# Kernel optimization log

Hardware: AMD Instinct MI355X
Metric: run time of the kernel (lower is better)

## Reference

```python
import jax, jax.numpy as jnp
import numpy as np
from jax import lax

GAMMA = 1.0
INF = 1000000.0  # matches the TF code's pseudo-infinity


def _pairwise_sq_dists(a, b):
    # ||a_i - b_j||^2 = ||a||^2 + ||b||^2 - 2 a.b ; avoids the [B,N,M,d] diff tensor
    a2 = jnp.sum(a * a, axis=-1)                      # (B, N)
    b2 = jnp.sum(b * b, axis=-1)                      # (B, M)
    ab = jnp.einsum('bnd,bmd->bnm', a, b)             # (B, N, M)
    return a2[:, :, None] + b2[:, None, :] - 2.0 * ab


def _soft_dtw(seq_a, seq_b, gamma):
    D = _pairwise_sq_dists(seq_a, seq_b)              # (B, N, M)
    B, N, M = D.shape
    dtype = D.dtype
    # row 0 of the DP table: R[0,0]=0, R[0,j>0]=INF
    row0 = jnp.full((B, M + 1), INF, dtype=dtype).at[:, 0].set(0.0)

    def row_step(prev_row, d_i):
        # prev_row: (B, M+1) = R[i-1, :]; d_i: (B, M) = D[:, i-1, :]
        def col_step(left, inputs):
            diag, up, d = inputs                      # each (B,)
            r = jnp.stack([diag, up, left], axis=-1)  # (B, 3)
            softmin = -gamma * jax.nn.logsumexp(-r / gamma, axis=-1)
            val = d + softmin
            return val, val
        left0 = jnp.full((B,), INF, dtype=dtype)      # R[i, 0] = INF
        xs = (prev_row[:, :-1].T, prev_row[:, 1:].T, d_i.T)  # scan over M
        _, vals = lax.scan(col_step, left0, xs)       # (M, B)
        new_row = jnp.concatenate([jnp.full((B, 1), INF, dtype=dtype), vals.T], axis=1)
        return new_row, None

    final_row, _ = lax.scan(row_step, row0, jnp.moveaxis(D, 1, 0))
    return final_row[:, -1]                           # R[N, M]


def setup_inputs() -> dict:
    key = jax.random.key(0)
    k1, k2 = jax.random.split(key)
    B, N, M, d = 128, 384, 384, 128
    seq_a = jax.random.normal(k1, (B, N, d), dtype=jnp.float32)
    seq_b = jax.random.normal(k2, (B, M, d), dtype=jnp.float32)
    return {"seq_a": seq_a, "seq_b": seq_b}


def reference(seq_a, seq_b):
    dist = _soft_dtw(seq_a, seq_b, GAMMA)
    return dist[:, None]                              # (B, 1)
```

## Files before the change

### kernel.cpp

```cpp
#include <hip/hip_runtime.h>
#include <stdint.h>

#define BATCH 128
#define SEQN  384
#define SEQM  384
#define DIM   128
#define KINF   1000000.0f
#define LOG2E  1.4426950408889634f
#define LN2    0.6931471805599453f
#define KINF2  (KINF * LOG2E)

#define RING    204
#define RSTRIDE 392

#define EXP2F(x) __builtin_amdgcn_exp2f(x)
#define LOG2F(x) __builtin_amdgcn_logf(x)

#define WG __HIP_MEMORY_SCOPE_WORKGROUP

typedef __attribute__((ext_vector_type(8))) short bf16x8;
typedef __attribute__((ext_vector_type(4))) float f32x4;

__device__ __forceinline__ unsigned short bf16_rne(float x) {
    uint32_t u = __float_as_uint(x);
    u += 0x7FFFu + ((u >> 16) & 1u);
    return (unsigned short)(u >> 16);
}
__device__ __forceinline__ uint32_t bf16_pair(float x, float y) {
    uint32_t ux = __float_as_uint(x); ux += 0x7FFFu + ((ux >> 16) & 1u);
    uint32_t uy = __float_as_uint(y); uy += 0x7FFFu + ((uy >> 16) & 1u);
    return (ux >> 16) | (uy & 0xFFFF0000u);
}

__device__ __forceinline__ float dpp_shfl_up1(float x) {
    return __int_as_float(__builtin_amdgcn_update_dpp(
        0, (int)__float_as_uint(x), 0x138 , 0xF, 0xF, false));
}

union frag_u { bf16x8 v; uint32_t u[4]; };

__global__ __launch_bounds__(512) void fused_dtw(
        const float* __restrict__ A, const float* __restrict__ B,
        float* __restrict__ out) {
    __shared__ __align__(16) unsigned short ring[RING * RSTRIDE];
    __shared__ __align__(16) float normA[SEQN];
    __shared__ int prod_done[16];
    __shared__ int cons_sl;

    const int bat  = blockIdx.x;
    const int tid  = threadIdx.x;
    const int wv   = tid >> 6;
    const int lane = tid & 63;

    if (tid < 16) prod_done[tid] = 0;
    if (tid == 16) cons_sl = -1;
    __syncthreads();

    if (wv == 4) {
        int g = 0;
        while (__hip_atomic_load(&cons_sl, __ATOMIC_ACQUIRE, WG) < 248) {
            __builtin_amdgcn_s_sleep(8);
            if (++g > (1 << 20)) break;
        }
        uint32_t pv = bf16_pair(KINF2, KINF2);
        #pragma unroll
        for (int c = 0; c < 4; c++) {
            uint32_t* p = (uint32_t*)&ring[(384 - RING + c) * RSTRIDE + 6 * lane];
            p[0] = pv; p[1] = pv; p[2] = pv;
        }
        if (lane == 0)
            __hip_atomic_fetch_add(&prod_done[12], 6, __ATOMIC_RELEASE, WG);
        return;
    }

    if (wv != 0) {
        const int pidx  = (wv < 4) ? (wv - 1) : (wv - 2);
        const int sbase = pidx * 4;
        const int l16 = lane & 15, q = lane >> 4;
        const float* __restrict__ Ab = A + (long)bat * SEQN * DIM;
        const float* __restrict__ Bb = B + (long)bat * SEQM * DIM;
        bool first = true;
        for (int k = 0; k < 12; k++) {
            if (k >= 6) {
                int thr = 32 * k - 110, g = 0;
                while (__hip_atomic_load(&cons_sl, __ATOMIC_ACQUIRE, WG) < thr) {
                    __builtin_amdgcn_s_sleep(2);
                    if (++g > (1 << 21)) break;
                }
            }
            frag_u bfrag[2][4];
            float bn[2];
            #pragma unroll
            for (int jg = 0; jg < 2; jg++) {
                const float* bp = Bb + (long)(32 * k + jg * 16 + l16) * DIM + q * 8;
                float s = 0.0f;
                #pragma unroll
                for (int kk = 0; kk < 4; kk++) {
                    float4 v0 = *(const float4*)(bp + kk * 32);
                    float4 v1 = *(const float4*)(bp + kk * 32 + 4);
                    bfrag[jg][kk].u[0] = bf16_pair(v0.x, v0.y);
                    bfrag[jg][kk].u[1] = bf16_pair(v0.z, v0.w);
                    bfrag[jg][kk].u[2] = bf16_pair(v1.x, v1.y);
                    bfrag[jg][kk].u[3] = bf16_pair(v1.z, v1.w);
                    s += v0.x*v0.x + v0.y*v0.y + v0.z*v0.z + v0.w*v0.w
                       + v1.x*v1.x + v1.y*v1.y + v1.z*v1.z + v1.w*v1.w;
                }
                s += __shfl_xor(s, 16, 64);
                s += __shfl_xor(s, 32, 64);
                bn[jg] = s;
            }
            float4 c0v[4], c1v[4];
            {
                const float* ap = Ab + (long)(sbase * 16 + l16) * DIM + q * 8;
                #pragma unroll
                for (int kk = 0; kk < 4; kk++) {
                    c0v[kk] = *(const float4*)(ap + kk * 32);
                    c1v[kk] = *(const float4*)(ap + kk * 32 + 4);
                }
            }
            #pragma unroll
            for (int s4 = 0; s4 < 4; s4++) {
                const int si = sbase + s4;
                float4 n0[4], n1[4];
                if (s4 < 3) {
                    const float* ap = Ab + (long)((si + 1) * 16 + l16) * DIM + q * 8;
                    #pragma unroll
                    for (int kk = 0; kk < 4; kk++) {
                        n0[kk] = *(const float4*)(ap + kk * 32);
                        n1[kk] = *(const float4*)(ap + kk * 32 + 4);
                    }
                }
                frag_u afr[4];
                #pragma unroll
                for (int kk = 0; kk < 4; kk++) {
                    afr[kk].u[0] = bf16_pair(c0v[kk].x, c0v[kk].y);
                    afr[kk].u[1] = bf16_pair(c0v[kk].z, c0v[kk].w);
                    afr[kk].u[2] = bf16_pair(c1v[kk].x, c1v[kk].y);
                    afr[kk].u[3] = bf16_pair(c1v[kk].z, c1v[kk].w);
                }
                if (first) {
                    float sa = 0.0f;
                    #pragma unroll
                    for (int kk = 0; kk < 4; kk++)
                        sa += c0v[kk].x*c0v[kk].x + c0v[kk].y*c0v[kk].y
                            + c0v[kk].z*c0v[kk].z + c0v[kk].w*c0v[kk].w
                            + c1v[kk].x*c1v[kk].x + c1v[kk].y*c1v[kk].y
                            + c1v[kk].z*c1v[kk].z + c1v[kk].w*c1v[kk].w;
                    sa += __shfl_xor(sa, 16, 64);
                    sa += __shfl_xor(sa, 32, 64);
                    if (q == 0) normA[si * 16 + l16] = sa;
                }
                f32x4 acc0 = {0.0f, 0.0f, 0.0f, 0.0f};
                f32x4 acc1 = {0.0f, 0.0f, 0.0f, 0.0f};
                #pragma unroll
                for (int kk = 0; kk < 4; kk++) {
                    acc0 = __builtin_amdgcn_mfma_f32_16x16x32_bf16(
                               afr[kk].v, bfrag[0][kk].v, acc0, 0, 0, 0);
                    acc1 = __builtin_amdgcn_mfma_f32_16x16x32_bf16(
                               afr[kk].v, bfrag[1][kk].v, acc1, 0, 0, 0);
                }
                if (first) asm volatile("s_waitcnt lgkmcnt(0)" ::: "memory");
                float4 an = *(const float4*)&normA[si * 16 + q * 4];
                #pragma unroll
                for (int jg = 0; jg < 2; jg++) {
                    int col  = 32 * k + jg * 16 + l16;
                    int slot = col >= RING ? col - RING : col;
                    f32x4 ac = jg ? acc1 : acc0;
                    ushort4 pk;
                    pk.x = bf16_rne((an.x + bn[jg] - 2.0f * ac[0]) * LOG2E);
                    pk.y = bf16_rne((an.y + bn[jg] - 2.0f * ac[1]) * LOG2E);
                    pk.z = bf16_rne((an.z + bn[jg] - 2.0f * ac[2]) * LOG2E);
                    pk.w = bf16_rne((an.w + bn[jg] - 2.0f * ac[3]) * LOG2E);
                    *(ushort4*)&ring[slot * RSTRIDE + si * 16 + q * 4] = pk;
                }
                if (s4 < 3) {
                    #pragma unroll
                    for (int kk = 0; kk < 4; kk++) { c0v[kk] = n0[kk]; c1v[kk] = n1[kk]; }
                }
            }
            first = false;
            if (lane == 0)
                __hip_atomic_fetch_add(&prod_done[k], 1, __ATOMIC_RELEASE, WG);
        }
        return;
    }

    const int t = lane;
    {
        int g = 0;
        while (__hip_atomic_load(&prod_done[0], __ATOMIC_ACQUIRE, WG) < 6)
            if (++g > (1 << 22)) break;
    }
    __builtin_amdgcn_s_setprio(1);
    const unsigned short* __restrict__ ringT = ring + 6 * t;

    float prev[6];
    #pragma unroll
    for (int r = 0; r < 6; r++) prev[r] = KINF2;

    uint3 dslot[4];
    #pragma unroll
    for (int j = 0; j < 4; j++) {
        int c = j - t;
        int cc = c < 0 ? 0 : c;
        dslot[j] = *(const uint3*)(ringT + (long)cc * RSTRIDE);
    }

    float rcv_up = KINF2, rcv_diag = KINF2;
    float lane0_diag = 0.0f;
    const bool isl0 = (t == 0);
    int kdone = 0;

#define UNPACK(d, w)                                                        \
    d[0] = __uint_as_float(w.x << 16);                                      \
    d[1] = __uint_as_float(w.x & 0xFFFF0000u);                              \
    d[2] = __uint_as_float(w.y << 16);                                      \
    d[3] = __uint_as_float(w.y & 0xFFFF0000u);                              \
    d[4] = __uint_as_float(w.z << 16);                                      \
    d[5] = __uint_as_float(w.z & 0xFFFF0000u);

#define COLPASS(dX, diag0, upseed, LEFTV, NEWV)                             \
    {                                                                       \
        float Bp = (upseed), Fp = 1.0f;                                     \
        float Bv[6], Fv[6];                                                 \
        _Pragma("unroll")                                                   \
        for (int r = 0; r < 6; r++) {                                       \
            float vd = (r == 0) ? (diag0) : LEFTV[r - 1];                   \
            float vl = LEFTV[r];                                            \
            float m3 = fminf(fminf(vd, vl), Bp);            \
            float al = EXP2F(m3 - Bp);                                      \
            float be = EXP2F(m3 - vd) + EXP2F(m3 - vl);                     \
            float Fr = __builtin_fmaf(al, Fp, be);                          \
            float Br = dX[r] + m3;                                          \
            Bv[r] = Br; Fv[r] = Fr;                                         \
            Bp = Br; Fp = Fr;                                               \
        }                                                                   \
        _Pragma("unroll")                                                   \
        for (int r = 0; r < 6; r++)                                         \
            NEWV[r] = Bv[r] - LOG2F(Fv[r]);                                 \
    }

#define SLOT(J, S)                                                          \
    {                                                                       \
        uint3 w = dslot[J];                                                 \
        {   int cn = (S) + 4 - t;                                           \
            int cc = cn < 0 ? 0 : (cn > 387 ? 387 : cn);                    \
            int sl = cc >= RING ? cc - RING : cc;                           \
            dslot[J] = *(const uint3*)(ringT + (long)sl * RSTRIDE);         \
        }                                                                   \
        float d6[6];                                                        \
        UNPACK(d6, w)                                                       \
        float dg = isl0 ? lane0_diag : rcv_diag;                            \
        float up = isl0 ? KINF2 : rcv_up;                                   \
        COLPASS(d6, dg, up, prev, prev)                                     \
        rcv_diag = rcv_up;                                                  \
        rcv_up = dpp_shfl_up1(prev[5]);                                     \
        lane0_diag = KINF2;                                                 \
    }

    for (int i = 0; i < 111; i++) {
        int kr = (4 * i + 7) >> 5;
        if (kr > 12) kr = 12;
        if (kr > kdone) {
            int g = 0;
            while (__hip_atomic_load(&prod_done[kr], __ATOMIC_ACQUIRE, WG) < 6)
                if (++g > (1 << 22)) break;
            kdone = kr;
        }
        SLOT(0, 4 * i)
        SLOT(1, 4 * i + 1)
        SLOT(2, 4 * i + 2)
        SLOT(3, 4 * i + 3)
        if ((i & 1) && t == 0)
            __hip_atomic_store(&cons_sl, 4 * i + 3,
                               __ATOMIC_RELEASE, WG);
    }
    SLOT(0, 444)
    SLOT(1, 445)
    SLOT(2, 446)
#undef SLOT
#undef COLPASS
#undef UNPACK

    if (t == 63) out[bat] = prev[5] * LN2;
}

extern "C" void kernel_launch(void* const* d_in, const int* in_sizes, int n_in,
                              void* d_out, int out_size, void* d_ws, size_t ws_size,
                              hipStream_t stream) {
    (void)in_sizes; (void)n_in; (void)out_size; (void)d_ws; (void)ws_size;
    const float* a = (const float*)d_in[0];
    const float* b = (const float*)d_in[1];
    float* out = (float*)d_out;

    fused_dtw<<<dim3(BATCH), dim3(512), 0, stream>>>(a, b, out);
}
```

Measured before the change: 184.0 us.

## Pack two batch items per workgroup with separate producer/consumer pipelines and smaller ring

```diff
diff --git a/kernel.cpp b/kernel.cpp
--- a/kernel.cpp
+++ b/kernel.cpp
@@ -10,7 +10,7 @@
 #define LN2    0.6931471805599453f
 #define KINF2  (KINF * LOG2E)
 
-#define RING    204
+#define RING    100
 #define RSTRIDE 392
 
 #define EXP2F(x) __builtin_amdgcn_exp2f(x)
@@ -42,48 +42,36 @@
 __global__ __launch_bounds__(512) void fused_dtw(
         const float* __restrict__ A, const float* __restrict__ B,
         float* __restrict__ out) {
-    __shared__ __align__(16) unsigned short ring[RING * RSTRIDE];
-    __shared__ __align__(16) float normA[SEQN];
-    __shared__ int prod_done[16];
-    __shared__ int cons_sl;
-
-    const int bat  = blockIdx.x;
+    __shared__ __align__(16) unsigned short ring[2][RING * RSTRIDE];
+    __shared__ __align__(16) float normA[2][SEQN];
+    __shared__ int prod_done[2][16];
+    __shared__ int cons_sl[2];
+
+    const int bx   = blockIdx.x;
     const int tid  = threadIdx.x;
     const int wv   = tid >> 6;
     const int lane = tid & 63;
 
-    if (tid < 16) prod_done[tid] = 0;
-    if (tid == 16) cons_sl = -1;
+    if (tid < 32) prod_done[tid >> 4][tid & 15] = 0;
+    if (tid == 32) cons_sl[0] = -1;
+    if (tid == 33) cons_sl[1] = -1;
     __syncthreads();
 
-    if (wv == 4) {
-        int g = 0;
-        while (__hip_atomic_load(&cons_sl, __ATOMIC_ACQUIRE, WG) < 248) {
-            __builtin_amdgcn_s_sleep(8);
-            if (++g > (1 << 20)) break;
-        }
-        uint32_t pv = bf16_pair(KINF2, KINF2);
-        #pragma unroll
-        for (int c = 0; c < 4; c++) {
-            uint32_t* p = (uint32_t*)&ring[(384 - RING + c) * RSTRIDE + 6 * lane];
-            p[0] = pv; p[1] = pv; p[2] = pv;
-        }
-        if (lane == 0)
-            __hip_atomic_fetch_add(&prod_done[12], 6, __ATOMIC_RELEASE, WG);
-        return;
-    }
-
-    if (wv != 0) {
-        const int pidx  = (wv < 4) ? (wv - 1) : (wv - 2);
-        const int sbase = pidx * 4;
+    const int b   = wv >> 2;
+    const int bat = 2 * bx + b;
+
+    if ((wv & 3) != 0) {
+        const int pidx  = (wv & 3) - 1;
+        const int sbase = pidx * 8;
         const int l16 = lane & 15, q = lane >> 4;
         const float* __restrict__ Ab = A + (long)bat * SEQN * DIM;
         const float* __restrict__ Bb = B + (long)bat * SEQM * DIM;
+        unsigned short* __restrict__ rng = ring[b];
         bool first = true;
         for (int k = 0; k < 12; k++) {
-            if (k >= 6) {
-                int thr = 32 * k - 110, g = 0;
-                while (__hip_atomic_load(&cons_sl, __ATOMIC_ACQUIRE, WG) < thr) {
+            if (k >= 3) {
+                int thr = 32 * k - 9, g = 0;
+                while (__hip_atomic_load(&cons_sl[b], __ATOMIC_ACQUIRE, WG) < thr) {
                     __builtin_amdgcn_s_sleep(2);
                     if (++g > (1 << 21)) break;
                 }
@@ -119,10 +107,10 @@
                 }
             }
             #pragma unroll
-            for (int s4 = 0; s4 < 4; s4++) {
-                const int si = sbase + s4;
+            for (int s8 = 0; s8 < 8; s8++) {
+                const int si = sbase + s8;
                 float4 n0[4], n1[4];
-                if (s4 < 3) {
+                if (s8 < 7) {
                     const float* ap = Ab + (long)((si + 1) * 16 + l16) * DIM + q * 8;
                     #pragma unroll
                     for (int kk = 0; kk < 4; kk++) {
@@ -148,7 +136,7 @@
                             + c1v[kk].z*c1v[kk].z + c1v[kk].w*c1v[kk].w;
                     sa += __shfl_xor(sa, 16, 64);
                     sa += __shfl_xor(sa, 32, 64);
-                    if (q == 0) normA[si * 16 + l16] = sa;
+                    if (q == 0) normA[b][si * 16 + l16] = sa;
                 }
                 f32x4 acc0 = {0.0f, 0.0f, 0.0f, 0.0f};
                 f32x4 acc1 = {0.0f, 0.0f, 0.0f, 0.0f};
@@ -160,27 +148,44 @@
                                afr[kk].v, bfrag[1][kk].v, acc1, 0, 0, 0);
                 }
                 if (first) asm volatile("s_waitcnt lgkmcnt(0)" ::: "memory");
-                float4 an = *(const float4*)&normA[si * 16 + q * 4];
+                float4 an = *(const float4*)&normA[b][si * 16 + q * 4];
                 #pragma unroll
                 for (int jg = 0; jg < 2; jg++) {
-                    int col  = 32 * k + jg * 16 + l16;
-                    int slot = col >= RING ? col - RING : col;
+                    int col = 32 * k + jg * 16 + l16;
+                    int sl  = col;
+                    if (sl >= 200) sl -= 200;
+                    if (sl >= 100) sl -= 100;
                     f32x4 ac = jg ? acc1 : acc0;
                     ushort4 pk;
                     pk.x = bf16_rne((an.x + bn[jg] - 2.0f * ac[0]) * LOG2E);
                     pk.y = bf16_rne((an.y + bn[jg] - 2.0f * ac[1]) * LOG2E);
                     pk.z = bf16_rne((an.z + bn[jg] - 2.0f * ac[2]) * LOG2E);
                     pk.w = bf16_rne((an.w + bn[jg] - 2.0f * ac[3]) * LOG2E);
-                    *(ushort4*)&ring[slot * RSTRIDE + si * 16 + q * 4] = pk;
-                }
-                if (s4 < 3) {
+                    *(ushort4*)&rng[sl * RSTRIDE + si * 16 + q * 4] = pk;
+                }
+                if (s8 < 7) {
                     #pragma unroll
                     for (int kk = 0; kk < 4; kk++) { c0v[kk] = n0[kk]; c1v[kk] = n1[kk]; }
                 }
             }
             first = false;
             if (lane == 0)
-                __hip_atomic_fetch_add(&prod_done[k], 1, __ATOMIC_RELEASE, WG);
+                __hip_atomic_fetch_add(&prod_done[b][k], 1, __ATOMIC_RELEASE, WG);
+        }
+        if (pidx == 0) {
+            int g = 0;
+            while (__hip_atomic_load(&cons_sl[b], __ATOMIC_ACQUIRE, WG) < 352) {
+                __builtin_amdgcn_s_sleep(8);
+                if (++g > (1 << 20)) break;
+            }
+            uint32_t pv = bf16_pair(KINF2, KINF2);
+            #pragma unroll
+            for (int c = 0; c < 4; c++) {
+                uint32_t* p = (uint32_t*)&rng[(84 + c) * RSTRIDE + 6 * lane];
+                p[0] = pv; p[1] = pv; p[2] = pv;
+            }
+            if (lane == 0)
+                __hip_atomic_store(&prod_done[b][12], 3, __ATOMIC_RELEASE, WG);
         }
         return;
     }
@@ -188,11 +193,11 @@
     const int t = lane;
     {
         int g = 0;
-        while (__hip_atomic_load(&prod_done[0], __ATOMIC_ACQUIRE, WG) < 6)
+        while (__hip_atomic_load(&prod_done[b][0], __ATOMIC_ACQUIRE, WG) < 3)
             if (++g > (1 << 22)) break;
     }
     __builtin_amdgcn_s_setprio(1);
-    const unsigned short* __restrict__ ringT = ring + 6 * t;
+    const unsigned short* __restrict__ ringT = ring[b] + 6 * t;
 
     float prev[6];
     #pragma unroll
@@ -245,9 +250,13 @@
         uint3 w = dslot[J];                                                 \
         {   int cn = (S) + 4 - t;                                           \
             int cc = cn < 0 ? 0 : (cn > 387 ? 387 : cn);                    \
-            int sl = cc >= RING ? cc - RING : cc;                           \
+            int sl = cc;                                                    \
+            if (sl >= 200) sl -= 200;                                       \
+            if (sl >= 100) sl -= 100;                                       \
             dslot[J] = *(const uint3*)(ringT + (long)sl * RSTRIDE);         \
         }                                                                   \
+        if (isl0)                             \
+            __hip_atomic_store(&cons_sl[b], (S), __ATOMIC_RELAXED, WG);     \
         float d6[6];                                                        \
         UNPACK(d6, w)                                                       \
         float dg = isl0 ? lane0_diag : rcv_diag;                            \
@@ -263,7 +272,7 @@
         if (kr > 12) kr = 12;
         if (kr > kdone) {
             int g = 0;
-            while (__hip_atomic_load(&prod_done[kr], __ATOMIC_ACQUIRE, WG) < 6)
+            while (__hip_atomic_load(&prod_done[b][kr], __ATOMIC_ACQUIRE, WG) < 3)
                 if (++g > (1 << 22)) break;
             kdone = kr;
         }
@@ -272,8 +281,7 @@
         SLOT(2, 4 * i + 2)
         SLOT(3, 4 * i + 3)
         if ((i & 1) && t == 0)
-            __hip_atomic_store(&cons_sl, 4 * i + 3,
-                               __ATOMIC_RELEASE, WG);
+            __hip_atomic_store(&cons_sl[b], 4 * i + 3, __ATOMIC_RELEASE, WG);
     }
     SLOT(0, 444)
     SLOT(1, 445)
@@ -293,5 +301,5 @@
     const float* b = (const float*)d_in[1];
     float* out = (float*)d_out;
 
-    fused_dtw<<<dim3(BATCH), dim3(512), 0, stream>>>(a, b, out);
-}
+    fused_dtw<<<dim3(BATCH / 2), dim3(512), 0, stream>>>(a, b, out);
+}
```

Measured after the change: 316.3 us. 72.0% more time.

## Carry soft-DTW cells as (base, mantissa) pairs to drop per-cell log2

Applied to the files above, without the earlier changes.

```diff
diff --git a/kernel.cpp b/kernel.cpp
--- a/kernel.cpp
+++ b/kernel.cpp
@@ -194,9 +194,9 @@
     __builtin_amdgcn_s_setprio(1);
     const unsigned short* __restrict__ ringT = ring + 6 * t;
 
-    float prev[6];
+    float prevB[6], prevF[6];
     #pragma unroll
-    for (int r = 0; r < 6; r++) prev[r] = KINF2;
+    for (int r = 0; r < 6; r++) { prevB[r] = KINF2; prevF[r] = 1.0f; }
 
     uint3 dslot[4];
     #pragma unroll
@@ -206,8 +206,9 @@
         dslot[j] = *(const uint3*)(ringT + (long)cc * RSTRIDE);
     }
 
-    float rcv_up = KINF2, rcv_diag = KINF2;
-    float lane0_diag = 0.0f;
+    float upB = KINF2, upF = 1.0f;
+    float dgB = KINF2, dgF = 1.0f;
+    float l0dB = 0.0f, l0dF = 1.0f;
     const bool isl0 = (t == 0);
     int kdone = 0;
 
@@ -219,25 +220,26 @@
     d[4] = __uint_as_float(w.z << 16);                                      \
     d[5] = __uint_as_float(w.z & 0xFFFF0000u);
 
-#define COLPASS(dX, diag0, upseed, LEFTV, NEWV)                             \
+#define COLPASS(dX, dgB_, dgF_, upB_, upF_)                                 \
     {                                                                       \
-        float Bp = (upseed), Fp = 1.0f;                                     \
-        float Bv[6], Fv[6];                                                 \
+        float Bp = (upB_), Fp = (upF_);                                     \
+        float cdB = (dgB_), cdF = (dgF_);                                   \
         _Pragma("unroll")                                                   \
         for (int r = 0; r < 6; r++) {                                       \
-            float vd = (r == 0) ? (diag0) : LEFTV[r - 1];                   \
-            float vl = LEFTV[r];                                            \
-            float m3 = fminf(fminf(vd, vl), Bp);            \
-            float al = EXP2F(m3 - Bp);                                      \
-            float be = EXP2F(m3 - vd) + EXP2F(m3 - vl);                     \
-            float Fr = __builtin_fmaf(al, Fp, be);                          \
+            float vdB = cdB, vdF = cdF;                                     \
+            float vlB = prevB[r], vlF = prevF[r];                           \
+            float m3 = fminf(fminf(vdB, vlB), Bp);          \
+            float Fr = EXP2F(m3 - Bp) * Fp;                                 \
+            Fr = __builtin_fmaf(EXP2F(m3 - vdB), vdF, Fr);                  \
+            Fr = __builtin_fmaf(EXP2F(m3 - vlB), vlF, Fr);                  \
             float Br = dX[r] + m3;                                          \
-            Bv[r] = Br; Fv[r] = Fr;                                         \
-            Bp = Br; Fp = Fr;                                               \
+            cdB = vlB; cdF = vlF;          \
+            uint32_t fb = __float_as_uint(Fr);                              \
+            int e = (int)(fb >> 23) - 127;                                  \
+            prevB[r] = Br - (float)e;                                       \
+            prevF[r] = __uint_as_float((fb & 0x007FFFFFu) | 0x3F800000u);   \
+            Bp = Br; Fp = Fr;           \
         }                                                                   \
-        _Pragma("unroll")                                                   \
-        for (int r = 0; r < 6; r++)                                         \
-            NEWV[r] = Bv[r] - LOG2F(Fv[r]);                                 \
     }
 
 #define SLOT(J, S)                                                          \
@@ -250,12 +252,15 @@
         }                                                                   \
         float d6[6];                                                        \
         UNPACK(d6, w)                                                       \
-        float dg = isl0 ? lane0_diag : rcv_diag;                            \
-        float up = isl0 ? KINF2 : rcv_up;                                   \
-        COLPASS(d6, dg, up, prev, prev)                                     \
-        rcv_diag = rcv_up;                                                  \
-        rcv_up = dpp_shfl_up1(prev[5]);                                     \
-        lane0_diag = KINF2;                                                 \
+        float dB = isl0 ? l0dB : dgB;                                       \
+        float dF = isl0 ? l0dF : dgF;                                       \
+        float uB = isl0 ? KINF2 : upB;                                      \
+        float uF = isl0 ? 1.0f  : upF;                                      \
+        COLPASS(d6, dB, dF, uB, uF)                                         \
+        dgB = upB; dgF = upF;                                               \
+        upB = dpp_shfl_up1(prevB[5]);                                       \
+        upF = dpp_shfl_up1(prevF[5]);                                       \
+        l0dB = KINF2; l0dF = 1.0f;                                          \
     }
 
     for (int i = 0; i < 111; i++) {
@@ -282,7 +287,7 @@
 #undef COLPASS
 #undef UNPACK
 
-    if (t == 63) out[bat] = prev[5] * LN2;
+    if (t == 63) out[bat] = (prevB[5] - LOG2F(prevF[5])) * LN2;
 }
 
 extern "C" void kernel_launch(void* const* d_in, const int* in_sizes, int n_in,
```

Result: slower. 199.3 us (+8.3%).
